# Kernel optimization log

Measured on AMD Instinct MI355X. Metric: run time of the kernel, lower is better.

Reference implementation:

```python
import jax, jax.numpy as jnp
import numpy as np

N_NODES = 8192
N_EDGES = 131072
EMB_NF = 256
IN_NODE_NF = 64
IN_EDGE_NF = 16


def setup_inputs() -> dict:
    key = jax.random.key(0)
    ks = jax.random.split(key, 8)
    node_emb = jax.random.normal(ks[0], (N_NODES, EMB_NF), dtype=jnp.float32)
    edge_emb = jax.random.normal(ks[1], (N_EDGES, EMB_NF), dtype=jnp.float32)
    # Linear head params (torch nn.Linear: y = x @ W.T + b)
    s = 1.0 / np.sqrt(EMB_NF)
    node_w = jax.random.uniform(ks[2], (IN_NODE_NF, EMB_NF), jnp.float32, -s, s)
    node_b = jax.random.uniform(ks[3], (IN_NODE_NF,), jnp.float32, -s, s)
    edge_w = jax.random.uniform(ks[4], (IN_EDGE_NF, EMB_NF), jnp.float32, -s, s)
    edge_b = jax.random.uniform(ks[5], (IN_EDGE_NF,), jnp.float32, -s, s)
    W = 0.5 * jnp.ones((1,), dtype=jnp.float32)
    b = 0.8 * jnp.ones((1,), dtype=jnp.float32)
    return {"node_emb": node_emb, "edge_emb": edge_emb,
            "node_w": node_w, "node_b": node_b,
            "edge_w": edge_w, "edge_b": edge_b,
            "W": W, "b": b}


def reference(node_emb, edge_emb, node_w, node_b, edge_w, edge_b, W, b):
    # Two linear decode heads
    recon_node_fs = node_emb @ node_w.T + node_b          # [N, in_node_nf]
    recon_edge_fs = edge_emb @ edge_w.T + edge_b          # [E, in_edge_nf]
    # Pairwise squared L2 distance: sum_d (x_i - x_j)^2 = |x_i|^2 + |x_j|^2 - 2 x_i.x_j
    sq = jnp.sum(node_emb * node_emb, axis=1)             # [N]
    d2 = sq[:, None] + sq[None, :] - 2.0 * (node_emb @ node_emb.T)  # [N, N]
    adj_pred = jax.nn.sigmoid(W[0] * d2 + b[0])           # [N, N]
    n = node_emb.shape[0]
    adj_pred = adj_pred * (1.0 - jnp.eye(n, dtype=adj_pred.dtype))  # remove self loops
    return (recon_node_fs, recon_edge_fs, adj_pred)
```

## Files before the change

kernel.cpp:

```cpp
#include <hip/hip_runtime.h>
#include <cstdint>
#include <cstddef>

#define NN 8192
#define NE 131072
#define EMB 256

typedef float f32x4 __attribute__((ext_vector_type(4)));
typedef __bf16 bf16x8 __attribute__((ext_vector_type(8)));

__device__ __forceinline__ unsigned short f2bf(float f) {
  unsigned u = __float_as_uint(f);
  u += 0x7fffu + ((u >> 16) & 1u);
  return (unsigned short)(u >> 16);
}

__device__ __forceinline__ void gload_lds16(const void* g, void* l) {
  __builtin_amdgcn_global_load_lds(
      (const __attribute__((address_space(1))) unsigned int*)g,
      (__attribute__((address_space(3))) unsigned int*)l, 16, 0, 0);
}

__global__ __launch_bounds__(256) void heads_kernel(const float* __restrict__ Xn,
                                                    const float* __restrict__ nw,
                                                    const float* __restrict__ nb,
                                                    const float* __restrict__ Xe,
                                                    const float* __restrict__ ew,
                                                    const float* __restrict__ eb,
                                                    float* __restrict__ node_out,
                                                    float* __restrict__ edge_out,
                                                    unsigned short* __restrict__ Xb,
                                                    float* __restrict__ sq) {
  __shared__ float lds[256 * 17];
  int tid = threadIdx.x;

  if (blockIdx.x < 512) {
    int e0 = blockIdx.x * 256;
    int lr = tid >> 2, lc = (tid & 3) * 4;

    float4 v[4];
    #pragma unroll
    for (int q = 0; q < 4; ++q)
      v[q] = *(const float4*)(Xe + (size_t)(e0 + lr + q * 64) * EMB + lc);

    float acc[16];
    #pragma unroll
    for (int o = 0; o < 16; ++o) acc[o] = 0.f;

    for (int kc = 0; kc < 16; ++kc) {
      __syncthreads();
      #pragma unroll
      for (int q = 0; q < 4; ++q) {
        float* d = &lds[(lr + q * 64) * 17 + lc];
        d[0] = v[q].x; d[1] = v[q].y; d[2] = v[q].z; d[3] = v[q].w;
      }
      __syncthreads();
      if (kc < 15) {
        #pragma unroll
        for (int q = 0; q < 4; ++q)
          v[q] = *(const float4*)(Xe + (size_t)(e0 + lr + q * 64) * EMB + (kc + 1) * 16 + lc);
      }
      const float* wk0 = ew + kc * 16;
      #pragma unroll
      for (int k = 0; k < 16; ++k) {
        float x = lds[tid * 17 + k];
        #pragma unroll
        for (int o = 0; o < 16; ++o)
          acc[o] = fmaf(x, wk0[(size_t)o * EMB + k], acc[o]);
      }
    }
    #pragma unroll
    for (int o = 0; o < 16; ++o) acc[o] += eb[o];
    float4* dst = (float4*)(edge_out + (size_t)(e0 + tid) * 16);
    dst[0] = make_float4(acc[0], acc[1], acc[2], acc[3]);
    dst[1] = make_float4(acc[4], acc[5], acc[6], acc[7]);
    dst[2] = make_float4(acc[8], acc[9], acc[10], acc[11]);
    dst[3] = make_float4(acc[12], acc[13], acc[14], acc[15]);
  } else {
    int n0 = (blockIdx.x - 512) * 16;
    int r = tid >> 4, g = tid & 15;
    float* xs = lds;

    float s = 0.f;
    #pragma unroll
    for (int kc = 0; kc < 4; ++kc) {
      float4 v = *(const float4*)(Xn + (size_t)(n0 + r) * EMB + kc * 64 + g * 4);
      *(float4*)(&xs[r * 260 + kc * 64 + g * 4]) = v;
      s += v.x * v.x + v.y * v.y + v.z * v.z + v.w * v.w;
      ushort4 b;
      b.x = f2bf(v.x); b.y = f2bf(v.y); b.z = f2bf(v.z); b.w = f2bf(v.w);
      *(ushort4*)(Xb + (size_t)(n0 + r) * EMB + kc * 64 + g * 4) = b;
    }
    s += __shfl_xor(s, 1); s += __shfl_xor(s, 2);
    s += __shfl_xor(s, 4); s += __shfl_xor(s, 8);
    if (g == 0) sq[n0 + r] = s;
    __syncthreads();

    int o0 = g * 4;
    float acc[4] = {0.f, 0.f, 0.f, 0.f};
    #pragma unroll 4
    for (int k = 0; k < 256; k += 4) {
      float4 x = *(const float4*)(&xs[r * 260 + k]);
      #pragma unroll
      for (int oo = 0; oo < 4; ++oo) {
        float4 wv = *(const float4*)(nw + (size_t)(o0 + oo) * EMB + k);
        acc[oo] = fmaf(x.x, wv.x, fmaf(x.y, wv.y, fmaf(x.z, wv.z, fmaf(x.w, wv.w, acc[oo]))));
      }
    }
    float4 o;
    o.x = acc[0] + nb[o0 + 0];
    o.y = acc[1] + nb[o0 + 1];
    o.z = acc[2] + nb[o0 + 2];
    o.w = acc[3] + nb[o0 + 3];
    *(float4*)(node_out + (size_t)(n0 + r) * 64 + o0) = o;
  }
}

__global__ __launch_bounds__(256) void adj_kernel(const unsigned short* __restrict__ Xb,
                                                  const float* __restrict__ sq,
                                                  const float* __restrict__ Wp,
                                                  const float* __restrict__ bp,
                                                  float* __restrict__ out) {
  __shared__ __align__(16) unsigned short As[128 * 64];
  __shared__ __align__(16) unsigned short Bs[128 * 64];

  int b   = blockIdx.x;
  int swz = (b & 7) * 512 + (b >> 3);
  int ti  = swz >> 6, tj = swz & 63;

  int tid  = threadIdx.x;
  int wave = tid >> 6, lane = tid & 63;
  int wr = (wave >> 1) * 64;
  int wc = (wave & 1) * 64;
  int l15 = lane & 15, lg = lane >> 4;

  f32x4 acc[4][4] = {};

  int r_base = tid >> 3;
  int cb     = (tid & 7) << 4;

  for (int kt = 0; kt < 4; ++kt) {
    #pragma unroll
    for (int it = 0; it < 4; ++it) {
      int r   = it * 32 + r_base;
      int cbs = cb ^ ((r & 7) << 4);
      int col = (kt << 6) + (cbs >> 1);
      const unsigned short* ga = Xb + (size_t)(ti * 128 + r) * EMB + col;
      const unsigned short* gb = Xb + (size_t)(tj * 128 + r) * EMB + col;
      gload_lds16(ga, (char*)As + it * 4096 + wave * 1024);
      gload_lds16(gb, (char*)Bs + it * 4096 + wave * 1024);
    }
    __syncthreads();
    #pragma unroll
    for (int ks = 0; ks < 2; ++ks) {
      bf16x8 af[4], bfr[4];
      #pragma unroll
      for (int m = 0; m < 4; ++m) {
        int rr = wr + m * 16 + l15;
        int bc = ((ks << 6) + (lg << 4)) ^ ((rr & 7) << 4);
        af[m] = *(const bf16x8*)((const char*)As + rr * 128 + bc);
      }
      #pragma unroll
      for (int n = 0; n < 4; ++n) {
        int rr = wc + n * 16 + l15;
        int bc = ((ks << 6) + (lg << 4)) ^ ((rr & 7) << 4);
        bfr[n] = *(const bf16x8*)((const char*)Bs + rr * 128 + bc);
      }
      #pragma unroll
      for (int m = 0; m < 4; ++m)
        #pragma unroll
        for (int n = 0; n < 4; ++n)
          acc[m][n] = __builtin_amdgcn_mfma_f32_16x16x32_bf16(af[m], bfr[n], acc[m][n], 0, 0, 0);
    }
    __syncthreads();
  }

  float W0 = Wp[0], b0 = bp[0];
  float w2 = -2.0f * W0;
  int col0 = tj * 128 + wc + l15;
  int row0 = ti * 128 + wr + (lg << 2);
  bool diag = (ti == tj);

  float aiW[16];
  #pragma unroll
  for (int m = 0; m < 4; ++m)
    #pragma unroll
    for (int rg = 0; rg < 4; ++rg)
      aiW[m * 4 + rg] = W0 * sq[row0 + m * 16 + rg];

  #pragma unroll
  for (int n = 0; n < 4; ++n) {
    int j = col0 + n * 16;
    float sjW = fmaf(W0, sq[j], b0);
    #pragma unroll
    for (int m = 0; m < 4; ++m) {
      #pragma unroll
      for (int rg = 0; rg < 4; ++rg) {
        float t = fmaf(w2, acc[m][n][rg], aiW[m * 4 + rg] + sjW);
        acc[m][n][rg] = __builtin_amdgcn_rcpf(1.0f + __expf(-t));
      }
      if (diag) {
        #pragma unroll
        for (int rg = 0; rg < 4; ++rg)
          if (row0 + m * 16 + rg == j) acc[m][n][rg] = 0.0f;
      }
      __builtin_nontemporal_store(acc[m][n],
          (f32x4*)(&out[(size_t)j * NN + row0 + m * 16]));
    }
  }
}

extern "C" void kernel_launch(void* const* d_in, const int* in_sizes, int n_in,
                              void* d_out, int out_size, void* d_ws, size_t ws_size,
                              hipStream_t stream) {
  const float* node_emb = (const float*)d_in[0];
  const float* edge_emb = (const float*)d_in[1];
  const float* node_w   = (const float*)d_in[2];
  const float* node_b   = (const float*)d_in[3];
  const float* edge_w   = (const float*)d_in[4];
  const float* edge_b   = (const float*)d_in[5];
  const float* Wp       = (const float*)d_in[6];
  const float* bp       = (const float*)d_in[7];

  float* out      = (float*)d_out;
  float* node_out = out;
  float* edge_out = out + (size_t)NN * 64;
  float* adj_out  = out + (size_t)NN * 64 + (size_t)NE * 16;

  unsigned short* Xb = (unsigned short*)d_ws;
  float* sq = (float*)((char*)d_ws + (size_t)NN * EMB * 2);

  heads_kernel<<<dim3(1024), dim3(256), 0, stream>>>(node_emb, node_w, node_b,
                                                     edge_emb, edge_w, edge_b,
                                                     node_out, edge_out, Xb, sq);
  adj_kernel<<<dim3(4096), dim3(256), 0, stream>>>(Xb, sq, Wp, bp, adj_out);
}
```

Measured before the change: 192.5 us.

## Move edge head into adjacency kernel, interleaving edge blocks with GEMM tiles

Splits the old combined heads kernel. The node prep (bf16 cast, squared norms, node head) now runs as its own small kernel, and the edge-head work moves into the adjacency kernel: every 9th block computes an edge-head tile, the other 8 compute adjacency tiles. The aim is to overlap the bandwidth-bound edge projection (reading 128 MB of edge embeddings) with the store-bound adjacency tiles, so the first phase no longer serialises it. The cost is a heterogeneous block mix that can unbalance occupancy, and a new tile-index mapping for the adjacency blocks.

```diff
diff --git a/kernel.cpp b/kernel.cpp
--- a/kernel.cpp
+++ b/kernel.cpp
@@ -21,21 +21,68 @@
       (__attribute__((address_space(3))) unsigned int*)l, 16, 0, 0);
 }
 
-__global__ __launch_bounds__(256) void heads_kernel(const float* __restrict__ Xn,
-                                                    const float* __restrict__ nw,
-                                                    const float* __restrict__ nb,
-                                                    const float* __restrict__ Xe,
-                                                    const float* __restrict__ ew,
-                                                    const float* __restrict__ eb,
-                                                    float* __restrict__ node_out,
-                                                    float* __restrict__ edge_out,
-                                                    unsigned short* __restrict__ Xb,
-                                                    float* __restrict__ sq) {
-  __shared__ float lds[256 * 17];
+__global__ __launch_bounds__(256) void node_prep_kernel(const float* __restrict__ X,
+                                                        const float* __restrict__ w,
+                                                        const float* __restrict__ bias,
+                                                        float* __restrict__ out,
+                                                        unsigned short* __restrict__ Xb,
+                                                        float* __restrict__ sq) {
+  __shared__ float xs[16 * 260];
   int tid = threadIdx.x;
-
-  if (blockIdx.x < 512) {
-    int e0 = blockIdx.x * 256;
+  int n0  = blockIdx.x * 16;
+  int r   = tid >> 4, g = tid & 15;
+
+  float s = 0.f;
+  #pragma unroll
+  for (int kc = 0; kc < 4; ++kc) {
+    float4 v = *(const float4*)(X + (size_t)(n0 + r) * EMB + kc * 64 + g * 4);
+    *(float4*)(&xs[r * 260 + kc * 64 + g * 4]) = v;
+    s += v.x * v.x + v.y * v.y + v.z * v.z + v.w * v.w;
+    ushort4 b;
+    b.x = f2bf(v.x); b.y = f2bf(v.y); b.z = f2bf(v.z); b.w = f2bf(v.w);
+    *(ushort4*)(Xb + (size_t)(n0 + r) * EMB + kc * 64 + g * 4) = b;
+  }
+  s += __shfl_xor(s, 1); s += __shfl_xor(s, 2);
+  s += __shfl_xor(s, 4); s += __shfl_xor(s, 8);
+  if (g == 0) sq[n0 + r] = s;
+  __syncthreads();
+
+  int o0 = g * 4;
+  float acc[4] = {0.f, 0.f, 0.f, 0.f};
+  #pragma unroll 4
+  for (int k = 0; k < 256; k += 4) {
+    float4 x = *(const float4*)(&xs[r * 260 + k]);
+    #pragma unroll
+    for (int oo = 0; oo < 4; ++oo) {
+      float4 wv = *(const float4*)(w + (size_t)(o0 + oo) * EMB + k);
+      acc[oo] = fmaf(x.x, wv.x, fmaf(x.y, wv.y, fmaf(x.z, wv.z, fmaf(x.w, wv.w, acc[oo]))));
+    }
+  }
+  float4 o;
+  o.x = acc[0] + bias[o0 + 0];
+  o.y = acc[1] + bias[o0 + 1];
+  o.z = acc[2] + bias[o0 + 2];
+  o.w = acc[3] + bias[o0 + 3];
+  *(float4*)(out + (size_t)(n0 + r) * 64 + o0) = o;
+}
+
+__global__ __launch_bounds__(256) void mega_kernel(const unsigned short* __restrict__ Xb,
+                                                   const float* __restrict__ sq,
+                                                   const float* __restrict__ Wp,
+                                                   const float* __restrict__ bp,
+                                                   float* __restrict__ adj_out,
+                                                   const float* __restrict__ Xe,
+                                                   const float* __restrict__ ew,
+                                                   const float* __restrict__ eb,
+                                                   float* __restrict__ edge_out) {
+  __shared__ __align__(16) char smem[32768];
+  int tid = threadIdx.x;
+  int b   = blockIdx.x;
+  int g   = b / 9, rem = b - g * 9;
+
+  if (rem == 8) {
+    float* lds = (float*)smem;
+    int e0 = g * 256;
     int lr = tid >> 2, lc = (tid & 3) * 4;
 
     float4 v[4];
@@ -76,59 +123,17 @@
     dst[1] = make_float4(acc[4], acc[5], acc[6], acc[7]);
     dst[2] = make_float4(acc[8], acc[9], acc[10], acc[11]);
     dst[3] = make_float4(acc[12], acc[13], acc[14], acc[15]);
-  } else {
-    int n0 = (blockIdx.x - 512) * 16;
-    int r = tid >> 4, g = tid & 15;
-    float* xs = lds;
-
-    float s = 0.f;
-    #pragma unroll
-    for (int kc = 0; kc < 4; ++kc) {
-      float4 v = *(const float4*)(Xn + (size_t)(n0 + r) * EMB + kc * 64 + g * 4);
-      *(float4*)(&xs[r * 260 + kc * 64 + g * 4]) = v;
-      s += v.x * v.x + v.y * v.y + v.z * v.z + v.w * v.w;
-      ushort4 b;
-      b.x = f2bf(v.x); b.y = f2bf(v.y); b.z = f2bf(v.z); b.w = f2bf(v.w);
-      *(ushort4*)(Xb + (size_t)(n0 + r) * EMB + kc * 64 + g * 4) = b;
-    }
-    s += __shfl_xor(s, 1); s += __shfl_xor(s, 2);
-    s += __shfl_xor(s, 4); s += __shfl_xor(s, 8);
-    if (g == 0) sq[n0 + r] = s;
-    __syncthreads();
-
-    int o0 = g * 4;
-    float acc[4] = {0.f, 0.f, 0.f, 0.f};
-    #pragma unroll 4
-    for (int k = 0; k < 256; k += 4) {
-      float4 x = *(const float4*)(&xs[r * 260 + k]);
-      #pragma unroll
-      for (int oo = 0; oo < 4; ++oo) {
-        float4 wv = *(const float4*)(nw + (size_t)(o0 + oo) * EMB + k);
-        acc[oo] = fmaf(x.x, wv.x, fmaf(x.y, wv.y, fmaf(x.z, wv.z, fmaf(x.w, wv.w, acc[oo]))));
-      }
-    }
-    float4 o;
-    o.x = acc[0] + nb[o0 + 0];
-    o.y = acc[1] + nb[o0 + 1];
-    o.z = acc[2] + nb[o0 + 2];
-    o.w = acc[3] + nb[o0 + 3];
-    *(float4*)(node_out + (size_t)(n0 + r) * 64 + o0) = o;
-  }
-}
-
-__global__ __launch_bounds__(256) void adj_kernel(const unsigned short* __restrict__ Xb,
-                                                  const float* __restrict__ sq,
-                                                  const float* __restrict__ Wp,
-                                                  const float* __restrict__ bp,
-                                                  float* __restrict__ out) {
-  __shared__ __align__(16) unsigned short As[128 * 64];
-  __shared__ __align__(16) unsigned short Bs[128 * 64];
-
-  int b   = blockIdx.x;
-  int swz = (b & 7) * 512 + (b >> 3);
-  int ti  = swz >> 6, tj = swz & 63;
-
-  int tid  = threadIdx.x;
+    return;
+  }
+
+  unsigned short* As = (unsigned short*)smem;
+  unsigned short* Bs = As + 128 * 64;
+
+  int adjid = g * 8 + rem;
+  int low3  = adjid & 7, q = adjid >> 3;
+  int ti = low3 * 8 + (q & 7);
+  int tj = ((q >> 6) & 7) * 8 + ((q >> 3) & 7);
+
   int wave = tid >> 6, lane = tid & 63;
   int wr = (wave >> 1) * 64;
   int wc = (wave & 1) * 64;
@@ -205,7 +210,7 @@
           if (row0 + m * 16 + rg == j) acc[m][n][rg] = 0.0f;
       }
       __builtin_nontemporal_store(acc[m][n],
-          (f32x4*)(&out[(size_t)j * NN + row0 + m * 16]));
+          (f32x4*)(&adj_out[(size_t)j * NN + row0 + m * 16]));
     }
   }
 }
@@ -230,8 +235,8 @@
   unsigned short* Xb = (unsigned short*)d_ws;
   float* sq = (float*)((char*)d_ws + (size_t)NN * EMB * 2);
 
-  heads_kernel<<<dim3(1024), dim3(256), 0, stream>>>(node_emb, node_w, node_b,
-                                                     edge_emb, edge_w, edge_b,
-                                                     node_out, edge_out, Xb, sq);
-  adj_kernel<<<dim3(4096), dim3(256), 0, stream>>>(Xb, sq, Wp, bp, adj_out);
-}
+  node_prep_kernel<<<dim3(512), dim3(256), 0, stream>>>(node_emb, node_w, node_b,
+                                                        node_out, Xb, sq);
+  mega_kernel<<<dim3(4608), dim3(256), 0, stream>>>(Xb, sq, Wp, bp, adj_out,
+                                                    edge_emb, edge_w, edge_b, edge_out);
+}
```

Result: faster. 180.6 us (-6.2%).
